# Optimization experiments

Measured on AMD Instinct MI355X. Metric: run time of the kernel, lower is better.

Reference implementation:

```python
import jax, jax.numpy as jnp
import numpy as np

B, T, F, H = 64, 2048, 256, 512


def setup_inputs() -> dict:
    key = jax.random.key(0)
    ks = jax.random.split(key, 8)
    s_ih = 1.0 / np.sqrt(H)
    return {
        "z": jax.random.normal(ks[0], (B, H), dtype=jnp.float32),
        "x": jax.random.normal(ks[1], (B, T, F), dtype=jnp.float32),
        "W_ih": jax.random.uniform(ks[2], (4 * H, F), minval=-s_ih, maxval=s_ih, dtype=jnp.float32),
        "W_hh": jax.random.uniform(ks[3], (4 * H, H), minval=-s_ih, maxval=s_ih, dtype=jnp.float32),
        "b_ih": jax.random.uniform(ks[4], (4 * H,), minval=-s_ih, maxval=s_ih, dtype=jnp.float32),
        "b_hh": jax.random.uniform(ks[5], (4 * H,), minval=-s_ih, maxval=s_ih, dtype=jnp.float32),
        "W_lin": jax.random.uniform(ks[6], (F, H), minval=-s_ih, maxval=s_ih, dtype=jnp.float32),
        "b_lin": jax.random.uniform(ks[7], (F,), minval=-s_ih, maxval=s_ih, dtype=jnp.float32),
    }


def _lstm_decode(z, x, W_ih, W_hh, b_ih, b_hh, W_lin, b_lin):
    # Teacher forcing: cell input at step t is x[:, t]. h0 = z, c0 = 0.
    # Precompute input projections for all timesteps in one GEMM: [T, B, 4H]
    x_t_major = jnp.swapaxes(x, 0, 1)  # [T, B, F]
    x_proj = jnp.einsum("tbf,gf->tbg", x_t_major, W_ih) + (b_ih + b_hh)
    h0 = z
    c0 = jnp.zeros_like(z)

    def step(carry, xp):
        h, c = carry
        gates = xp + h @ W_hh.T  # [B, 4H]
        i, f, g, o = jnp.split(gates, 4, axis=-1)  # PyTorch gate order: i,f,g,o
        i = jax.nn.sigmoid(i)
        f = jax.nn.sigmoid(f)
        g = jnp.tanh(g)
        o = jax.nn.sigmoid(o)
        c_new = f * c + i * g
        h_new = o * jnp.tanh(c_new)
        out_t = h_new @ W_lin.T + b_lin  # [B, F]
        return (h_new, c_new), out_t

    _, outs = jax.lax.scan(step, (h0, c0), x_proj)  # outs: [T, B, F]
    return jnp.swapaxes(outs, 0, 1)  # [B, T, F]


def reference(z, x, W_ih, W_hh, b_ih, b_hh, W_lin, b_lin):
    return _lstm_decode(z, x, W_ih, W_hh, b_ih, b_hh, W_lin, b_lin)
```

## Files before the change

kernel.cpp:

```cpp
#include <hip/hip_runtime.h>
#include <hip/hip_bf16.h>

#define B_   64
#define T_   2048
#define F_   256
#define H_   512
#define GB   4
#define GG   8
#define NWG  (GB*GG)
#define PAYD 4096

typedef __attribute__((ext_vector_type(8))) short bfrag;
typedef __attribute__((ext_vector_type(4))) int   int4v;
typedef __attribute__((ext_vector_type(4))) float f32x4;
typedef __attribute__((ext_vector_type(4))) float float4_t;

__device__ __forceinline__ float fsig(float x)  { return 1.0f / (1.0f + __expf(-x)); }
__device__ __forceinline__ float ftanh(float x) { return 2.0f / (1.0f + __expf(-2.0f * x)) - 1.0f; }
__device__ __forceinline__ short f2bf(float f) {
  __hip_bfloat16 h = __float2bfloat16(f);
  return __builtin_bit_cast(short, h);
}

__device__ __forceinline__ int gload4_cc(const void* p) {
  int r;
  asm volatile("global_load_dword %0, %1, off sc0 sc1" : "=v"(r) : "v"(p));
  return r;
}
__device__ __forceinline__ int4v gload16_cc(const void* p) {
  int4v r;
  asm volatile("global_load_dwordx4 %0, %1, off sc0 sc1" : "=v"(r) : "v"(p));
  return r;
}
__device__ __forceinline__ void gstore4_cc(void* p, int d) {
  asm volatile("global_store_dword %0, %1, off sc0 sc1" :: "v"(p), "v"(d));
}
__device__ __forceinline__ int gload_flag(const void* p) {
  int r;
  asm volatile("global_load_dword %0, %1, off sc0 sc1\n\ts_waitcnt vmcnt(0)"
               : "=v"(r) : "v"(p) : "memory");
  return r;
}
__device__ __forceinline__ void vm_drain() {
  asm volatile("s_waitcnt vmcnt(0)" ::: "memory");
  __builtin_amdgcn_sched_barrier(0);
}

__global__ void lstm_init(const float* __restrict__ z, int* __restrict__ pay,
                          int* __restrict__ flags) {
  int i = blockIdx.x * blockDim.x + threadIdx.x;
  if (i < GB * 16) flags[i] = 0;
  int g  = i >> 12;
  int p  = i & 4095;
  int j  = p >> 8;
  int pr = p & 255;
  int row = 16 * g + j;
  int lo = (int)((unsigned)(unsigned short)f2bf(z[(size_t)row * H_ + 2 * pr])
         | ((unsigned)(unsigned short)f2bf(z[(size_t)row * H_ + 2 * pr + 1]) << 16));
  pay[(size_t)g * PAYD + p] = lo;
}

__global__ void e_b16(const int* r) {
  const int l = threadIdx.x;
  for (int it = 0; it < 4096; ++it) {
    int v[16];
    #pragma unroll
    for (int j = 0; j < 16; ++j)
      v[j] = gload4_cc(r + l + j * 64 + (it & 1) * 1024);
    vm_drain();
    #pragma unroll
    for (int j = 0; j < 16; ++j) asm volatile("" :: "v"(v[j]));
  }
}
__global__ void e_b4(const int* r) {
  const int l = threadIdx.x;
  for (int it = 0; it < 4096; ++it) {
    int4v v[4];
    #pragma unroll
    for (int j = 0; j < 4; ++j)
      v[j] = gload16_cc((const char*)r + l * 16 + j * 1024 + (it & 1) * 4096);
    vm_drain();
    #pragma unroll
    for (int j = 0; j < 4; ++j)
      asm volatile("" :: "v"(v[j][0]), "v"(v[j][1]), "v"(v[j][2]), "v"(v[j][3]));
  }
}

__global__ void __launch_bounds__(256, 1)
lstm_persist(const float* __restrict__ x,
             const float* __restrict__ Wih,  const float* __restrict__ Whh,
             const float* __restrict__ bih,  const float* __restrict__ bhh,
             const float* __restrict__ Wlin, const float* __restrict__ blin,
             float* __restrict__ out, int* __restrict__ pay,
             int* __restrict__ flags)
{
  __shared__ char smem[49152];

  const int wg  = blockIdx.x;
  const int b   = wg >> 3;
  const int k   = wg & 7;
  const int tid = threadIdx.x;
  const int wv  = tid >> 6;
  const int l   = tid & 63;
  const int l16 = l & 15;
  const int qq  = l >> 4;
  const int swz = (l16 & 7) << 4;
  const int m4  = qq << 2;

  {
    const int oc = tid >> 3;
    const float* src = Wlin + (size_t)(32 * k + oc) * H_ + (tid & 7) * 64;
    char* dst = smem + 16384 + oc * 1024;
    #pragma unroll
    for (int i = 0; i < 8; ++i) {
      bfrag tmp;
      #pragma unroll
      for (int e = 0; e < 8; ++e) tmp[e] = f2bf(src[i * 8 + e]);
      *(int4v*)(dst + ((((tid & 7) * 128) + i * 16) ^ ((oc & 7) << 4))) =
          __builtin_bit_cast(int4v, tmp);
    }
  }

  bfrag WH[4][16]; bfrag WI[4][8]; float bs[4];
  #pragma unroll
  for (int q = 0; q < 4; ++q) {
    const int grow = q * H_ + k * 64 + wv * 16 + l16;
    #pragma unroll
    for (int kt = 0; kt < 16; ++kt) {
      const float* s = Whh + (size_t)grow * H_ + kt * 32 + qq * 8;
      bfrag w;
      #pragma unroll
      for (int e = 0; e < 8; ++e) w[e] = f2bf(s[e]);
      WH[q][kt] = w;
    }
    #pragma unroll
    for (int kt = 0; kt < 8; ++kt) {
      const float* s = Wih + (size_t)grow * F_ + kt * 32 + qq * 8;
      bfrag w;
      #pragma unroll
      for (int e = 0; e < 8; ++e) w[e] = f2bf(s[e]);
      WI[q][kt] = w;
    }
    bs[q] = bih[grow] + bhh[grow];
  }
  const float blc = (wv < 2) ? blin[32 * k + 16 * wv + l16] : 0.f;

  float c4[4] = {0.f, 0.f, 0.f, 0.f};
  __syncthreads();

  const int* myflags = flags + b * 16;
  const int prow = tid >> 4;
  const int pcol = tid & 15;

  for (int t = 0; t < T_; ++t) {
    if (t > 0) {
      while (true) {
        int v = gload_flag(&myflags[l & 7]);
        if (__all(v >= t)) break;
        __builtin_amdgcn_s_sleep(1);
      }
      __builtin_amdgcn_sched_barrier(0);
    }

    const char* pbase = (const char*)(pay + (size_t)((t & 1) * GB + b) * PAYD) + tid * 64;
    int4v pv4[4];
    #pragma unroll
    for (int i = 0; i < 4; ++i) pv4[i] = gload16_cc(pbase + i * 16);

    f32x4 acc[4] = {{0,0,0,0},{0,0,0,0},{0,0,0,0},{0,0,0,0}};
    {
      const float* xr = x + ((size_t)(16 * b + l16) * T_ + t) * F_ + qq * 8;
      #pragma unroll
      for (int kt = 0; kt < 8; ++kt) {
        float4_t xa = *(const float4_t*)(xr + kt * 32);
        float4_t xb = *(const float4_t*)(xr + kt * 32 + 4);
        bfrag a;
        #pragma unroll
        for (int e = 0; e < 4; ++e) { a[e] = f2bf(xa[e]); a[4 + e] = f2bf(xb[e]); }
        #pragma unroll
        for (int q = 0; q < 4; ++q)
          acc[q] = __builtin_amdgcn_mfma_f32_16x16x32_bf16(a, WI[q][kt], acc[q], 0, 0, 0);
      }
    }
    vm_drain();
    __syncthreads();

    {
      char* rowbase = smem + prow * 1024;
      #pragma unroll
      for (int i = 0; i < 4; ++i)
        *(int4v*)(rowbase + ((pcol * 64 + i * 16) ^ ((prow & 7) << 4))) = pv4[i];
    }
    __syncthreads();

    f32x4 oacc = {blc, blc, blc, blc};
    #pragma unroll
    for (int kt = 0; kt < 16; ++kt) {
      bfrag a = *(const bfrag*)(smem + l16 * 1024 + ((kt * 64 + qq * 16) ^ swz));
      #pragma unroll
      for (int q = 0; q < 4; ++q)
        acc[q] = __builtin_amdgcn_mfma_f32_16x16x32_bf16(a, WH[q][kt], acc[q], 0, 0, 0);
      if (wv < 2) {
        bfrag wl = *(const bfrag*)(smem + 16384 + (16 * wv + l16) * 1024 +
                                   ((kt * 64 + qq * 16) ^ swz));
        oacc = __builtin_amdgcn_mfma_f32_16x16x32_bf16(a, wl, oacc, 0, 0, 0);
      }
    }

    int* ps = pay + (size_t)(((t + 1) & 1) * GB + b) * PAYD;
    #pragma unroll
    for (int r = 0; r < 4; ++r) {
      float iv = fsig(acc[0][r] + bs[0]);
      float fv = fsig(acc[1][r] + bs[1]);
      float gv = ftanh(acc[2][r] + bs[2]);
      float ov = fsig(acc[3][r] + bs[3]);
      float cn = fv * c4[r] + iv * gv;
      c4[r] = cn;
      float hn = ov * ftanh(cn);
      int hb = (int)(unsigned short)f2bf(hn);
      int pu = __shfl_xor(hb, 1);
      if ((l16 & 1) == 0) {
        int packed = (hb & 0xffff) | (pu << 16);
        gstore4_cc(ps + (m4 + r) * 256 + (32 * k + 8 * wv + (l16 >> 1)), packed);
      }
    }
    vm_drain();
    __syncthreads();
    if (tid == 0)
      gstore4_cc((void*)&flags[b * 16 + k], t + 1);

    if (t > 0 && wv < 2) {
      #pragma unroll
      for (int r = 0; r < 4; ++r)
        out[(size_t)(16 * b + m4 + r) * T_ * F_ + (size_t)(t - 1) * F_ +
            32 * k + 16 * wv + l16] = oacc[r];
    }
  }

  {
    while (true) {
      int v = gload_flag(&myflags[l & 7]);
      if (__all(v >= T_)) break;
      __builtin_amdgcn_s_sleep(1);
    }
    __builtin_amdgcn_sched_barrier(0);

    const char* pbase = (const char*)(pay + (size_t)((T_ & 1) * GB + b) * PAYD) + tid * 64;
    int4v pv4[4];
    #pragma unroll
    for (int i = 0; i < 4; ++i) pv4[i] = gload16_cc(pbase + i * 16);
    vm_drain();
    __syncthreads();
    {
      char* rowbase = smem + prow * 1024;
      #pragma unroll
      for (int i = 0; i < 4; ++i)
        *(int4v*)(rowbase + ((pcol * 64 + i * 16) ^ ((prow & 7) << 4))) = pv4[i];
    }
    __syncthreads();

    if (wv < 2) {
      f32x4 oacc = {blc, blc, blc, blc};
      #pragma unroll
      for (int kt = 0; kt < 16; ++kt) {
        bfrag a  = *(const bfrag*)(smem + l16 * 1024 + ((kt * 64 + qq * 16) ^ swz));
        bfrag wl = *(const bfrag*)(smem + 16384 + (16 * wv + l16) * 1024 +
                                   ((kt * 64 + qq * 16) ^ swz));
        oacc = __builtin_amdgcn_mfma_f32_16x16x32_bf16(a, wl, oacc, 0, 0, 0);
      }
      #pragma unroll
      for (int r = 0; r < 4; ++r)
        out[(size_t)(16 * b + m4 + r) * T_ * F_ + (size_t)(T_ - 1) * F_ +
            32 * k + 16 * wv + l16] = oacc[r];
    }
  }
}

extern "C" void kernel_launch(void* const* d_in, const int* in_sizes, int n_in,
                              void* d_out, int out_size, void* d_ws, size_t ws_size,
                              hipStream_t stream) {
  const float* z    = (const float*)d_in[0];
  const float* x    = (const float*)d_in[1];
  const float* Wih  = (const float*)d_in[2];
  const float* Whh  = (const float*)d_in[3];
  const float* bih  = (const float*)d_in[4];
  const float* bhh  = (const float*)d_in[5];
  const float* Wlin = (const float*)d_in[6];
  const float* blin = (const float*)d_in[7];
  float* out = (float*)d_out;

  int* pay   = (int*)d_ws;
  int* flags = (int*)((char*)d_ws + 192 * 1024);
  int* preg  = (int*)((char*)d_ws + 256 * 1024);

  lstm_init<<<64, 256, 0, stream>>>(z, pay, flags);
  e_b16<<<1, 64, 0, stream>>>(preg);
  e_b4 <<<1, 64, 0, stream>>>(preg);
  lstm_persist<<<NWG, 256, 0, stream>>>(x, Wih, Whh, bih, bhh, Wlin, blin, out,
                                        pay, flags);
}
```

Measured before the change: 16.71 ms.

## Use per-wave flags, vectorized payload stores, and defer output GEMM past flag signal

Replaces the per-workgroup barrier plus single flag with one flag per wavefront, so each wave signals its h slice as soon as its own stores drain, and pollers check 32 flags. Changes the payload layout so each lane writes its four rows with one 16-byte store instead of four 4-byte stores. Moves the output-projection MFMA after the flag signal so it overlaps other groups' work instead of sitting on the recurrence critical path. Drops the two unused probe kernels e_b16 and e_b4 from the launch. The trade-off is more flag polling traffic and scattered 4-byte LDS writes when unpacking the payload.

```diff
diff --git a/kernel.cpp b/kernel.cpp
--- a/kernel.cpp
+++ b/kernel.cpp
@@ -22,15 +22,13 @@
   return __builtin_bit_cast(short, h);
 }
 
-__device__ __forceinline__ int gload4_cc(const void* p) {
-  int r;
-  asm volatile("global_load_dword %0, %1, off sc0 sc1" : "=v"(r) : "v"(p));
-  return r;
-}
 __device__ __forceinline__ int4v gload16_cc(const void* p) {
   int4v r;
   asm volatile("global_load_dwordx4 %0, %1, off sc0 sc1" : "=v"(r) : "v"(p));
   return r;
+}
+__device__ __forceinline__ void gstore16_cc(void* p, int4v d) {
+  asm volatile("global_store_dwordx4 %0, %1, off sc0 sc1" :: "v"(p), "v"(d));
 }
 __device__ __forceinline__ void gstore4_cc(void* p, int d) {
   asm volatile("global_store_dword %0, %1, off sc0 sc1" :: "v"(p), "v"(d));
@@ -49,41 +47,15 @@
 __global__ void lstm_init(const float* __restrict__ z, int* __restrict__ pay,
                           int* __restrict__ flags) {
   int i = blockIdx.x * blockDim.x + threadIdx.x;
-  if (i < GB * 16) flags[i] = 0;
+  if (i < GB * 32) flags[i] = 0;
   int g  = i >> 12;
   int p  = i & 4095;
-  int j  = p >> 8;
-  int pr = p & 255;
+  int P  = p >> 4;
+  int j  = p & 15;
   int row = 16 * g + j;
-  int lo = (int)((unsigned)(unsigned short)f2bf(z[(size_t)row * H_ + 2 * pr])
-         | ((unsigned)(unsigned short)f2bf(z[(size_t)row * H_ + 2 * pr + 1]) << 16));
-  pay[(size_t)g * PAYD + p] = lo;
-}
-
-__global__ void e_b16(const int* r) {
-  const int l = threadIdx.x;
-  for (int it = 0; it < 4096; ++it) {
-    int v[16];
-    #pragma unroll
-    for (int j = 0; j < 16; ++j)
-      v[j] = gload4_cc(r + l + j * 64 + (it & 1) * 1024);
-    vm_drain();
-    #pragma unroll
-    for (int j = 0; j < 16; ++j) asm volatile("" :: "v"(v[j]));
-  }
-}
-__global__ void e_b4(const int* r) {
-  const int l = threadIdx.x;
-  for (int it = 0; it < 4096; ++it) {
-    int4v v[4];
-    #pragma unroll
-    for (int j = 0; j < 4; ++j)
-      v[j] = gload16_cc((const char*)r + l * 16 + j * 1024 + (it & 1) * 4096);
-    vm_drain();
-    #pragma unroll
-    for (int j = 0; j < 4; ++j)
-      asm volatile("" :: "v"(v[j][0]), "v"(v[j][1]), "v"(v[j][2]), "v"(v[j][3]));
-  }
+  int lo = (int)((unsigned)(unsigned short)f2bf(z[(size_t)row * H_ + 2 * P])
+         | ((unsigned)(unsigned short)f2bf(z[(size_t)row * H_ + 2 * P + 1]) << 16));
+  pay[(size_t)g * PAYD + P * 16 + j] = lo;
 }
 
 __global__ void __launch_bounds__(256, 1)
@@ -148,14 +120,13 @@
   float c4[4] = {0.f, 0.f, 0.f, 0.f};
   __syncthreads();
 
-  const int* myflags = flags + b * 16;
-  const int prow = tid >> 4;
-  const int pcol = tid & 15;
+  const int* myflags = flags + b * 32;
+  const int  myPair  = 32 * k + 8 * wv + (l16 >> 1);
 
   for (int t = 0; t < T_; ++t) {
     if (t > 0) {
       while (true) {
-        int v = gload_flag(&myflags[l & 7]);
+        int v = (l < 32) ? gload_flag(&myflags[l]) : t;
         if (__all(v >= t)) break;
         __builtin_amdgcn_s_sleep(1);
       }
@@ -165,7 +136,7 @@
     const char* pbase = (const char*)(pay + (size_t)((t & 1) * GB + b) * PAYD) + tid * 64;
     int4v pv4[4];
     #pragma unroll
-    for (int i = 0; i < 4; ++i) pv4[i] = gload16_cc(pbase + i * 16);
+    for (int a = 0; a < 4; ++a) pv4[a] = gload16_cc(pbase + a * 16);
 
     f32x4 acc[4] = {{0,0,0,0},{0,0,0,0},{0,0,0,0},{0,0,0,0}};
     {
@@ -185,29 +156,26 @@
     vm_drain();
     __syncthreads();
 
-    {
-      char* rowbase = smem + prow * 1024;
-      #pragma unroll
-      for (int i = 0; i < 4; ++i)
-        *(int4v*)(rowbase + ((pcol * 64 + i * 16) ^ ((prow & 7) << 4))) = pv4[i];
-    }
-    __syncthreads();
-
-    f32x4 oacc = {blc, blc, blc, blc};
+    #pragma unroll
+    for (int a = 0; a < 4; ++a) {
+      #pragma unroll
+      for (int i = 0; i < 4; ++i) {
+        const int j = 4 * a + i;
+        *(int*)(smem + j * 1024 + ((tid * 4) ^ ((j & 7) << 4))) = pv4[a][i];
+      }
+    }
+    __syncthreads();
+
     #pragma unroll
     for (int kt = 0; kt < 16; ++kt) {
       bfrag a = *(const bfrag*)(smem + l16 * 1024 + ((kt * 64 + qq * 16) ^ swz));
       #pragma unroll
       for (int q = 0; q < 4; ++q)
         acc[q] = __builtin_amdgcn_mfma_f32_16x16x32_bf16(a, WH[q][kt], acc[q], 0, 0, 0);
-      if (wv < 2) {
-        bfrag wl = *(const bfrag*)(smem + 16384 + (16 * wv + l16) * 1024 +
-                                   ((kt * 64 + qq * 16) ^ swz));
-        oacc = __builtin_amdgcn_mfma_f32_16x16x32_bf16(a, wl, oacc, 0, 0, 0);
-      }
     }
 
     int* ps = pay + (size_t)(((t + 1) & 1) * GB + b) * PAYD;
+    int hb[4];
     #pragma unroll
     for (int r = 0; r < 4; ++r) {
       float iv = fsig(acc[0][r] + bs[0]);
@@ -216,30 +184,43 @@
       float ov = fsig(acc[3][r] + bs[3]);
       float cn = fv * c4[r] + iv * gv;
       c4[r] = cn;
-      float hn = ov * ftanh(cn);
-      int hb = (int)(unsigned short)f2bf(hn);
-      int pu = __shfl_xor(hb, 1);
-      if ((l16 & 1) == 0) {
-        int packed = (hb & 0xffff) | (pu << 16);
-        gstore4_cc(ps + (m4 + r) * 256 + (32 * k + 8 * wv + (l16 >> 1)), packed);
-      }
+      hb[r] = (int)(unsigned short)f2bf(ov * ftanh(cn));
+    }
+    {
+      int4v pk;
+      #pragma unroll
+      for (int r = 0; r < 4; ++r) {
+        int pu = __shfl_xor(hb[r], 1);
+        pk[r] = (hb[r] & 0xffff) | (pu << 16);
+      }
+      if ((l16 & 1) == 0)
+        gstore16_cc(ps + myPair * 16 + m4, pk);
     }
     vm_drain();
-    __syncthreads();
-    if (tid == 0)
-      gstore4_cc((void*)&flags[b * 16 + k], t + 1);
-
-    if (t > 0 && wv < 2) {
-      #pragma unroll
-      for (int r = 0; r < 4; ++r)
-        out[(size_t)(16 * b + m4 + r) * T_ * F_ + (size_t)(t - 1) * F_ +
-            32 * k + 16 * wv + l16] = oacc[r];
+    if (l == 0)
+      gstore4_cc((void*)&flags[b * 32 + k * 4 + wv], t + 1);
+
+    if (wv < 2) {
+      f32x4 oacc = {blc, blc, blc, blc};
+      #pragma unroll
+      for (int kt = 0; kt < 16; ++kt) {
+        bfrag a  = *(const bfrag*)(smem + l16 * 1024 + ((kt * 64 + qq * 16) ^ swz));
+        bfrag wl = *(const bfrag*)(smem + 16384 + (16 * wv + l16) * 1024 +
+                                   ((kt * 64 + qq * 16) ^ swz));
+        oacc = __builtin_amdgcn_mfma_f32_16x16x32_bf16(a, wl, oacc, 0, 0, 0);
+      }
+      if (t > 0) {
+        #pragma unroll
+        for (int r = 0; r < 4; ++r)
+          out[(size_t)(16 * b + m4 + r) * T_ * F_ + (size_t)(t - 1) * F_ +
+              32 * k + 16 * wv + l16] = oacc[r];
+      }
     }
   }
 
   {
     while (true) {
-      int v = gload_flag(&myflags[l & 7]);
+      int v = (l < 32) ? gload_flag(&myflags[l]) : T_;
       if (__all(v >= T_)) break;
       __builtin_amdgcn_s_sleep(1);
     }
@@ -248,14 +229,16 @@
     const char* pbase = (const char*)(pay + (size_t)((T_ & 1) * GB + b) * PAYD) + tid * 64;
     int4v pv4[4];
     #pragma unroll
-    for (int i = 0; i < 4; ++i) pv4[i] = gload16_cc(pbase + i * 16);
+    for (int a = 0; a < 4; ++a) pv4[a] = gload16_cc(pbase + a * 16);
     vm_drain();
     __syncthreads();
-    {
-      char* rowbase = smem + prow * 1024;
-      #pragma unroll
-      for (int i = 0; i < 4; ++i)
-        *(int4v*)(rowbase + ((pcol * 64 + i * 16) ^ ((prow & 7) << 4))) = pv4[i];
+    #pragma unroll
+    for (int a = 0; a < 4; ++a) {
+      #pragma unroll
+      for (int i = 0; i < 4; ++i) {
+        const int j = 4 * a + i;
+        *(int*)(smem + j * 1024 + ((tid * 4) ^ ((j & 7) << 4))) = pv4[a][i];
+      }
     }
     __syncthreads();
 
@@ -291,11 +274,8 @@
 
   int* pay   = (int*)d_ws;
   int* flags = (int*)((char*)d_ws + 192 * 1024);
-  int* preg  = (int*)((char*)d_ws + 256 * 1024);
 
   lstm_init<<<64, 256, 0, stream>>>(z, pay, flags);
-  e_b16<<<1, 64, 0, stream>>>(preg);
-  e_b4 <<<1, 64, 0, stream>>>(preg);
   lstm_persist<<<NWG, 256, 0, stream>>>(x, Wih, Whh, bih, bhh, Wlin, blin, out,
                                         pay, flags);
 }
```

Result: faster. 14.24 ms (-14.8%).
